# Performance work log

Measured on AMD Instinct MI355X. Metric: run time of the kernel, lower is better.

## Reference

```python
import jax, jax.numpy as jnp
import numpy as np

K = 16
N_BLOCKS = 3
EPS = 1e-5  # nn.BatchNorm2d default eps


def setup_inputs() -> dict:
    key = jax.random.key(0)
    ks = jax.random.split(key, 4)
    b, n, c_out = 8, 4096, 64
    s = 0.1
    return {
        "xyz": jax.random.normal(ks[0], (b, 3, n), dtype=jnp.float32),
        "w1": jax.random.normal(ks[1], (c_out, 3), dtype=jnp.float32) * s,
        "b1": jnp.zeros((c_out,), jnp.float32),
        "w2": jax.random.normal(ks[2], (c_out, c_out), dtype=jnp.float32) * s,
        "b2": jnp.zeros((c_out,), jnp.float32),
        "gamma": jnp.ones((c_out,), jnp.float32),
        "beta": jnp.zeros((c_out,), jnp.float32),
    }


def _forward(xyz, w1, b1, w2, b2, gamma, beta):
    pts = jnp.transpose(xyz, (0, 2, 1))  # (b, n, 3)
    sq = jnp.sum(pts * pts, axis=-1)     # (b, n)
    # dist[b, i, j] = ||pts[b, j] - pts[b, i]||^2  (gram trick, avoids (b,n,n,3))
    dist = sq[:, :, None] + sq[:, None, :] - 2.0 * jnp.einsum('bic,bjc->bij', pts, pts)
    # NOTE: torch.topk defaults to LARGEST values -- faithful to the source code,
    # which (perhaps unintentionally) selects the k+1 FARTHEST points.
    _, idx = jax.lax.top_k(dist, K + 1)  # (b, n, K+1)
    idx = idx[:, :, 1:]                  # drop first, dilation=1 -> (b, n, K)
    # gather neighbor coords: nbr[b, i, j] = pts[b, idx[b, i, j]]
    nbr = jax.vmap(lambda p, i: p[i])(pts, idx)      # (b, n, K, 3)
    rel = nbr - pts[:, :, None, :]                    # relative coords (b, n, K, 3)
    g = jnp.transpose(rel, (0, 3, 2, 1))              # (b, 3, K, n)
    for blk in range(N_BLOCKS):
        w, bb = (w1, b1) if blk == 0 else (w2, b2)
        g = jnp.einsum('oc,bckn->bokn', w, g) + bb[None, :, None, None]
        if blk == N_BLOCKS - 1:
            return jnp.max(g, axis=2)                 # (b, c_out, n)
        # self.bn is the BatchNorm2d module (truthy) so BN is always applied;
        # fresh torch module is in training mode -> batch statistics.
        mu = jnp.mean(g, axis=(0, 2, 3), keepdims=True)
        var = jnp.mean((g - mu) ** 2, axis=(0, 2, 3), keepdims=True)
        g = (g - mu) * jax.lax.rsqrt(var + EPS)
        g = g * gamma[None, :, None, None] + beta[None, :, None, None]
        g = jax.nn.relu(g)


def reference(xyz, w1, b1, w2, b2, gamma, beta):
    return _forward(xyz, w1, b1, w2, b2, gamma, beta)
```

## Files before the change

### kernel.cpp

```cpp
#include <hip/hip_runtime.h>

typedef unsigned int u32;
typedef unsigned short u16;
typedef unsigned long long u64;
typedef __attribute__((ext_vector_type(8))) short bf16x8;
typedef __attribute__((ext_vector_type(4))) float f32x4;

#define REL_OFF   0
#define PTS4_OFF  1572864
#define ACC_OFF   1703936
#define EXT_OFF   1705360
#define EXT_END   1713552


__device__ __forceinline__ u32 bfh(float v){
  u32 x = __float_as_uint(v);
  return (x + 0x7FFFu + ((x >> 16) & 1u)) >> 16;
}
__device__ __forceinline__ void split2(float v, u16* hh, u16* hl){
  u32 h = bfh(v);
  float hif = __uint_as_float(h << 16);
  u32 l = bfh(v - hif);
  *hh = (u16)h; *hl = (u16)l;
}
__device__ __forceinline__ u32 cvt_pk_bf16(float a, float b){
  u32 r;
  asm("v_cvt_pk_bf16_f32 %0, %1, %2" : "=v"(r) : "v"(a), "v"(b));
  return r;
}

template<int N>
__device__ __forceinline__ float dpp_ror_f(float x){
  int r = __builtin_amdgcn_update_dpp(__float_as_int(x), __float_as_int(x),
                                      0x120 + N, 0xf, 0xf, false);
  return __int_as_float(r);
}
__device__ __forceinline__ float row_sum16(float x){
  x += dpp_ror_f<1>(x);
  x += dpp_ror_f<2>(x);
  x += dpp_ror_f<4>(x);
  x += dpp_ror_f<8>(x);
  return x;
}
__device__ __forceinline__ float row_max16(float x){
  x = fmaxf(x, dpp_ror_f<1>(x));
  x = fmaxf(x, dpp_ror_f<2>(x));
  x = fmaxf(x, dpp_ror_f<4>(x));
  x = fmaxf(x, dpp_ror_f<8>(x));
  return x;
}

__global__ __launch_bounds__(256) void prep_kernel(const float* __restrict__ xyz,
                                                   float4* __restrict__ pts4,
                                                   float* __restrict__ mom,
                                                   const float* __restrict__ w2,
                                                   u16* __restrict__ w2h,
                                                   u16* __restrict__ w2l,
                                                   float* __restrict__ gsum32,
                                                   float* __restrict__ gsq32,
                                                   int do_w2){
#pragma clang fp contract(off)
  int g = blockIdx.x*256 + threadIdx.x;
  if (g < 16) mom[g] = 0.0f;
  if (do_w2){
    if (g < 4096) split2(w2[g], &w2h[g], &w2l[g]);
    if (g < 2048) gsum32[g] = 0.0f;
    else if (g < 4096) gsq32[g-2048] = 0.0f;
  }
  int b = g >> 12, n = g & 4095;
  const float* xb = xyz + (size_t)b*12288;
  float x = xb[n], y = xb[4096+n], z = xb[8192+n];
  float sq = (x*x + y*y) + z*z;
  pts4[g] = make_float4(x,y,z,sq);
}

__global__ void w2prep_kernel(const float* __restrict__ w2,
                              u16* __restrict__ w2h, u16* __restrict__ w2l,
                              float* __restrict__ gsum32, float* __restrict__ gsq32){
  int i = blockIdx.x*256 + threadIdx.x;
  split2(w2[i], &w2h[i], &w2l[i]);
  if (i < 2048) gsum32[i] = 0.0f; else gsq32[i-2048] = 0.0f;
}

template<int N>
__device__ __forceinline__ void chain_insert_n(double* s, double key){
  #pragma unroll
  for (int t = N-1; t >= 1; --t)
    s[t] = fmax(s[t], fmin(s[t-1], key));
  s[0] = fmax(s[0], key);
}

__global__ __launch_bounds__(256) void knn_kernel(const float4* __restrict__ pts4,
                                                  float* __restrict__ rel,
                                                  float* __restrict__ mom){
#pragma clang fp contract(off)
  __shared__ double ring[4352];
  __shared__ float bmom[16];
  __shared__ u32 gate[32];
  u32* lA = (u32*)ring;
  u16* lB = (u16*)((char*)ring + 18048);
  const int tid  = threadIdx.x;
  const int lane = tid & 63;
  const int wave = tid >> 6;
  const int q    = lane & 31;
  const int h    = lane >> 5;
  const int sp   = wave*2 + h;
  const int blk  = blockIdx.x;
  const int b    = blk >> 7;
  const int q0   = (blk & 127) << 5;
  const float4* __restrict__ P = pts4 + ((size_t)b << 12);
  const float4* __restrict__ C = P + (sp << 9);
  const float4 me = P[q0 + q];
  if (tid < 16) bmom[tid] = 0.0f;
  if (tid < 32) gate[tid] = 0u;
  __syncthreads();

  double s[17];
  #pragma unroll
  for (int i=0;i<17;i++) s[i] = 0.0;
  const int base = tid*17;
  const int jg0 = sp << 9;
  u32 wr = 0, rd = 0;
  double pD_ = 0.0;
  const double kinv = 1.52587890625e-05;

  #define KEY48(u, J) ({                                              \
    float dot_ = (me.x*c[(u)].x + me.y*c[(u)].y) + me.z*c[(u)].z;     \
    float d_   = (me.w + c[(u)].w) - 2.0f*dot_;                       \
    u32 ub_ = __float_as_uint(d_);                                    \
    ub_ ^= ((u32)(((int)ub_) >> 31) | 0x80000000u);                   \
    (double)ub_ * 65536.0 + (double)(4095 - (J)); })

  {
    float4 c[8];
    #pragma unroll
    for (int u=0;u<8;u++) c[u] = C[u];
    chain_insert_n<1>(s, KEY48(0, jg0+0));
    chain_insert_n<2>(s, KEY48(1, jg0+1));
    chain_insert_n<3>(s, KEY48(2, jg0+2));
    chain_insert_n<4>(s, KEY48(3, jg0+3));
    chain_insert_n<5>(s, KEY48(4, jg0+4));
    chain_insert_n<6>(s, KEY48(5, jg0+5));
    chain_insert_n<7>(s, KEY48(6, jg0+6));
    chain_insert_n<8>(s, KEY48(7, jg0+7));
  }
  {
    float4 c[8];
    #pragma unroll
    for (int u=0;u<8;u++) c[u] = C[8+u];
    chain_insert_n< 9>(s, KEY48(0, jg0+ 8));
    chain_insert_n<10>(s, KEY48(1, jg0+ 9));
    chain_insert_n<11>(s, KEY48(2, jg0+10));
    chain_insert_n<12>(s, KEY48(3, jg0+11));
    chain_insert_n<13>(s, KEY48(4, jg0+12));
    chain_insert_n<14>(s, KEY48(5, jg0+13));
    chain_insert_n<15>(s, KEY48(6, jg0+14));
    chain_insert_n<16>(s, KEY48(7, jg0+15));
  }
  {
    float4 c[8];
    #pragma unroll
    for (int u=0;u<8;u++) c[u] = C[16+u];
    #pragma unroll
    for (int u=0;u<8;u++) chain_insert_n<17>(s, KEY48(u, jg0+16+u));
  }

  u32 lastpub = (u32)(s[16] * kinv);
  atomicMax(&gate[q], lastpub);
  u32 ob = lastpub;

  #define INSERT_STEP() {                                        \
    bool act = rd != wr;                                         \
    double key = act ? pD_ : 0.0;                                \
    rd += act;                                                   \
    pD_ = ring[base + (int)(rd & 15u)];                          \
    if (__any(key > s[16])) chain_insert_n<17>(s, key);          \
  }

  for (int g8 = 24; g8 < 512; g8 += 8){
    if (__any((int)(wr - rd) >= 9)){
      do { INSERT_STEP(); } while (__any(rd != wr));
      ob = (u32)(s[16] * kinv);
      if (ob > lastpub){ atomicMax(&gate[q], ob); lastpub = ob; }
    }
    float4 c[8];
    #pragma unroll
    for (int u=0;u<8;u++) c[u] = C[g8 + u];
    const u32 mb = max(gate[q], ob);
    const u32 ib = (mb >> 31) ? (mb ^ 0x80000000u) : ~mb;
    const float gmin = __uint_as_float(ib);
    const u32 wr0 = wr;
    #pragma unroll
    for (int u=0;u<8;u++){
      const int j = jg0 + g8 + u;
      float dot = (me.x*c[u].x + me.y*c[u].y) + me.z*c[u].z;
      float d   = (me.w + c[u].w) - 2.0f*dot;
      if (d >= gmin){
        u32 ub = __float_as_uint(d);
        ub ^= ((u32)(((int)ub) >> 31) | 0x80000000u);
        ring[base + (int)(wr & 15u)] = (double)ub * 65536.0 + (double)(4095 - j);
        wr++;
      }
    }
    if (wr != wr0) pD_ = ring[base + (int)(rd & 15u)];
  }
  while (__any(rd != wr)) INSERT_STEP();
  #undef INSERT_STEP
  #undef KEY48

  __syncthreads();
  #pragma unroll
  for (int i=0;i<17;i++){
    const int o = (sp*17 + i)*33 + q;
    u32 hi = (u32)(s[i] * kinv);
    u32 lo = (u32)(s[i] - (double)hi * 65536.0);
    lA[o] = hi;
    lB[o] = (u16)lo;
  }
  __syncthreads();

  {
    const int mq  = tid >> 3;
    const int sub = tid & 7;
    const float4 qp = P[q0 + mq];
    float* __restrict__ ro = rel + (size_t)((b << 12) + q0 + mq) * 48;
    float sm0=0,sm1=0,sm2=0,sm3=0,sm4=0,sm5=0,sm6=0,sm7=0,sm8=0;
    int p = 0;
    for (int r=0;r<17;r++){
      const int idx = (sub*17 + p)*33 + mq;
      u64 mine = ((u64)lA[idx] << 16) | lB[idx];
      u64 kmax = mine;
      #pragma unroll
      for (int off=1; off<8; off<<=1){
        u64 o2 = __shfl_xor(kmax, off);
        kmax = (o2 > kmax) ? o2 : kmax;
      }
      p += (mine == kmax);
      if (r > 0 && sub == 0){
        const int j = 4095 - (int)(u32)(kmax & 0xFFFFull);
        const float4 nb = P[j];
        const float rx = nb.x - qp.x;
        const float ry = nb.y - qp.y;
        const float rz = nb.z - qp.z;
        ro[(r-1)*3+0] = rx; ro[(r-1)*3+1] = ry; ro[(r-1)*3+2] = rz;
        sm0 += rx; sm1 += ry; sm2 += rz;
        sm3 += rx*rx; sm4 += rx*ry; sm5 += rx*rz;
        sm6 += ry*ry; sm7 += ry*rz; sm8 += rz*rz;
      }
    }
    #pragma unroll
    for (int off=8; off<64; off<<=1){
      sm0 += __shfl_xor(sm0, off); sm1 += __shfl_xor(sm1, off); sm2 += __shfl_xor(sm2, off);
      sm3 += __shfl_xor(sm3, off); sm4 += __shfl_xor(sm4, off); sm5 += __shfl_xor(sm5, off);
      sm6 += __shfl_xor(sm6, off); sm7 += __shfl_xor(sm7, off); sm8 += __shfl_xor(sm8, off);
    }
    if (lane == 0){
      atomicAdd(&bmom[0], sm0); atomicAdd(&bmom[1], sm1); atomicAdd(&bmom[2], sm2);
      atomicAdd(&bmom[3], sm3); atomicAdd(&bmom[4], sm4); atomicAdd(&bmom[5], sm5);
      atomicAdd(&bmom[6], sm6); atomicAdd(&bmom[7], sm7); atomicAdd(&bmom[8], sm8);
    }
  }
  __syncthreads();
  if (tid < 9) atomicAdd(&mom[tid], bmom[tid]);
}

__device__ __noinline__ void stats1_to_lds(int o, const float* __restrict__ mom,
    const float* __restrict__ w1, const float* __restrict__ b1,
    const float* __restrict__ gamma, const float* __restrict__ beta,
    float* a1){
  const float Minv = 1.0f / 524288.0f;
  float m0 = mom[0]*Minv, m1 = mom[1]*Minv, m2 = mom[2]*Minv;
  float cxx = mom[3]*Minv - m0*m0;
  float cxy = mom[4]*Minv - m0*m1;
  float cxz = mom[5]*Minv - m0*m2;
  float cyy = mom[6]*Minv - m1*m1;
  float cyz = mom[7]*Minv - m1*m2;
  float czz = mom[8]*Minv - m2*m2;
  float wx = w1[o*3+0], wy = w1[o*3+1], wz = w1[o*3+2];
  float mu  = wx*m0 + wy*m1 + wz*m2 + b1[o];
  float var = wx*wx*cxx + wy*wy*cyy + wz*wz*czz
            + 2.0f*(wx*wy*cxy + wx*wz*cxz + wy*wz*cyz);
  float istd = rsqrtf(var + 1e-5f);
  float sc = gamma[o]*istd;
  float t1 = beta[o] - mu*sc;
  a1[o*4+0] = wx*sc;
  a1[o*4+1] = wy*sc;
  a1[o*4+2] = wz*sc;
  a1[o*4+3] = fmaf(sc, b1[o], t1);
}

__device__ __forceinline__ void stage_H_core(int e, int half,
    float rx, float ry, float rz, const float* a1, u16* Hh, u16* Hl){
  const float4* A1 = (const float4*)a1;
  const int ch0 = half*32;
  #pragma unroll
  for (int i=0;i<32;i+=4){
    float g[4];
    #pragma unroll
    for (int r2=0;r2<4;r2++){
      float4 a = A1[ch0+i+r2];
      float t = fmaf(a.x, rx, fmaf(a.y, ry, fmaf(a.z, rz, a.w)));
      g[r2] = fmaxf(t, 0.0f);
    }
    u32 h01 = cvt_pk_bf16(g[0], g[1]);
    u32 h23 = cvt_pk_bf16(g[2], g[3]);
    float l0 = g[0] - __uint_as_float(h01 << 16);
    float l1 = g[1] - __uint_as_float(h01 & 0xFFFF0000u);
    float l2 = g[2] - __uint_as_float(h23 << 16);
    float l3 = g[3] - __uint_as_float(h23 & 0xFFFF0000u);
    u32 l01 = cvt_pk_bf16(l0, l1);
    u32 l23 = cvt_pk_bf16(l2, l3);
    *(uint2*)&Hh[e*72 + ch0 + i] = make_uint2(h01, h23);
    *(uint2*)&Hl[e*72 + ch0 + i] = make_uint2(l01, l23);
  }
}

#define MFMA6(dst, b_h0, b_h1, b_l0, b_l1)                                   \
  dst = __builtin_amdgcn_mfma_f32_16x16x32_bf16(aH0, b_h0, dst, 0,0,0);      \
  dst = __builtin_amdgcn_mfma_f32_16x16x32_bf16(aH1, b_h1, dst, 0,0,0);      \
  dst = __builtin_amdgcn_mfma_f32_16x16x32_bf16(aH0, b_l0, dst, 0,0,0);      \
  dst = __builtin_amdgcn_mfma_f32_16x16x32_bf16(aH1, b_l1, dst, 0,0,0);      \
  dst = __builtin_amdgcn_mfma_f32_16x16x32_bf16(aL0, b_h0, dst, 0,0,0);      \
  dst = __builtin_amdgcn_mfma_f32_16x16x32_bf16(aL1, b_h1, dst, 0,0,0);

#define LOAD_W_FRAGS()                                                        \
  const int rA = (wave*16 + col)*64 + quad*8;                                 \
  bf16x8 aH0 = *(const bf16x8*)&w2h[rA];                                      \
  bf16x8 aH1 = *(const bf16x8*)&w2h[rA+32];                                   \
  bf16x8 aL0 = *(const bf16x8*)&w2l[rA];                                      \
  bf16x8 aL1 = *(const bf16x8*)&w2l[rA+32];

__global__ __launch_bounds__(256) void pass2_mfma(
    const float* __restrict__ rel,
    const float* __restrict__ mom, const float* __restrict__ w1,
    const float* __restrict__ b1, const float* __restrict__ gamma,
    const float* __restrict__ beta,
    const u16* __restrict__ w2h, const u16* __restrict__ w2l,
    const float* __restrict__ b2,
    float* __restrict__ gsum32, float* __restrict__ gsq32){
  __shared__ alignas(16) u16 Hh[128*72], Hl[128*72];
  __shared__ float a1s[256];
  const int tid = threadIdx.x, blk = blockIdx.x;
  const int e = tid>>1, half = tid&1;
  size_t eg = (size_t)blk*128 + e;
  const float rx = rel[eg*3+0], ry = rel[eg*3+1], rz = rel[eg*3+2];
  if (tid < 64) stats1_to_lds(tid, mom, w1, b1, gamma, beta, a1s);
  __syncthreads();
  stage_H_core(e, half, rx, ry, rz, (const float*)a1s, Hh, Hl);
  __syncthreads();
  const int lane = tid & 63, wave = tid >> 6;
  const int col = lane & 15, quad = lane >> 4;
  LOAD_W_FRAGS()
  float b2v[4];
  #pragma unroll
  for (int r=0;r<4;r++) b2v[r] = b2[wave*16 + quad*4 + r];
  float ssum[4] = {0,0,0,0}, ssq[4] = {0,0,0,0};
  #pragma unroll
  for (int nt=0; nt<8; nt++){
    const int offB = (nt*16 + col)*72 + quad*8;
    bf16x8 bH0 = *(const bf16x8*)&Hh[offB];
    bf16x8 bH1 = *(const bf16x8*)&Hh[offB+32];
    bf16x8 bL0 = *(const bf16x8*)&Hl[offB];
    bf16x8 bL1 = *(const bf16x8*)&Hl[offB+32];
    f32x4 a = {0.f,0.f,0.f,0.f};
    MFMA6(a, bH0, bH1, bL0, bL1)
    #pragma unroll
    for (int r=0;r<4;r++){
      float t = a[r] + b2v[r];
      ssum[r] += t; ssq[r] += t*t;
    }
  }
  #pragma unroll
  for (int r=0;r<4;r++){
    ssum[r] = row_sum16(ssum[r]);
    ssq[r]  = row_sum16(ssq[r]);
  }
  if (col == 0){
    const int st = (blk & 31)*64;
    #pragma unroll
    for (int r=0;r<4;r++){
      int ch = wave*16 + quad*4 + r;
      atomicAdd(&gsum32[st+ch], ssum[r]);
      atomicAdd(&gsq32[st+ch],  ssq[r]);
    }
  }
}

__global__ __launch_bounds__(256) void pass3_mfma(
    const float* __restrict__ rel,
    const float* __restrict__ mom, const float* __restrict__ w1,
    const float* __restrict__ b1, const float* __restrict__ gamma,
    const float* __restrict__ beta,
    const u16* __restrict__ w2h, const u16* __restrict__ w2l,
    const float* __restrict__ b2,
    const float* __restrict__ gsum32, const float* __restrict__ gsq32,
    float* __restrict__ out){
  __shared__ alignas(16) u16 Hh[128*72], Hl[128*72];
  __shared__ float a1s[256];
  __shared__ float s2s[64], c2s[64];
  const int tid = threadIdx.x, blk = blockIdx.x;
  const int e = tid>>1, half = tid&1;
  size_t eg = (size_t)blk*128 + e;
  const float rx = rel[eg*3+0], ry = rel[eg*3+1], rz = rel[eg*3+2];
  if (tid < 64){
    stats1_to_lds(tid, mom, w1, b1, gamma, beta, a1s);
  } else if (tid < 128){
    const int o = tid - 64;
    float s = 0.f, q = 0.f;
    #pragma unroll
    for (int i=0;i<32;i++){ s += gsum32[i*64+o]; q += gsq32[i*64+o]; }
    const float Minv = 1.0f / 524288.0f;
    float mu  = s*Minv;
    float var = q*Minv - mu*mu;
    float istd = rsqrtf(var + 1e-5f);
    float sc = gamma[o]*istd;
    float t2 = beta[o] - mu*sc;
    s2s[o] = sc;
    c2s[o] = fmaf(sc, b2[o], t2);
  }
  __syncthreads();
  stage_H_core(e, half, rx, ry, rz, (const float*)a1s, Hh, Hl);
  __syncthreads();
  const int lane = tid & 63, wave = tid >> 6;
  const int col = lane & 15, quad = lane >> 4;
  LOAD_W_FRAGS()
  float s2v[4], c2v[4], b2v[4];
  #pragma unroll
  for (int r=0;r<4;r++){
    int ch = wave*16 + quad*4 + r;
    s2v[r] = s2s[ch]; c2v[r] = c2s[ch]; b2v[r] = b2[ch];
  }
  f32x4 acc[8];
  #pragma unroll
  for (int nt=0; nt<8; nt++){
    const int offB = (nt*16 + col)*72 + quad*8;
    bf16x8 bH0 = *(const bf16x8*)&Hh[offB];
    bf16x8 bH1 = *(const bf16x8*)&Hh[offB+32];
    bf16x8 bL0 = *(const bf16x8*)&Hl[offB];
    bf16x8 bL1 = *(const bf16x8*)&Hl[offB+32];
    f32x4 a = {0.f,0.f,0.f,0.f};
    MFMA6(a, bH0, bH1, bL0, bL1)
    acc[nt] = a;
  }
  __syncthreads();
  #pragma unroll
  for (int nt=0; nt<8; nt++){
    const int eo = nt*16 + col;
    const int ch0 = wave*16 + quad*4;
    float h0, h1, h2, h3;
    {
      float g0 = acc[nt][0] + b2v[0];
      float g1 = acc[nt][1] + b2v[1];
      float g2 = acc[nt][2] + b2v[2];
      float g3 = acc[nt][3] + b2v[3];
      h0 = fmaxf(fmaf(g0, s2v[0], c2v[0]), 0.0f);
      h1 = fmaxf(fmaf(g1, s2v[1], c2v[1]), 0.0f);
      h2 = fmaxf(fmaf(g2, s2v[2], c2v[2]), 0.0f);
      h3 = fmaxf(fmaf(g3, s2v[3], c2v[3]), 0.0f);
    }
    u32 h01 = cvt_pk_bf16(h0, h1);
    u32 h23 = cvt_pk_bf16(h2, h3);
    float l0 = h0 - __uint_as_float(h01 << 16);
    float l1 = h1 - __uint_as_float(h01 & 0xFFFF0000u);
    float l2 = h2 - __uint_as_float(h23 << 16);
    float l3 = h3 - __uint_as_float(h23 & 0xFFFF0000u);
    u32 l01 = cvt_pk_bf16(l0, l1);
    u32 l23 = cvt_pk_bf16(l2, l3);
    *(uint2*)&Hh[eo*72 + ch0] = make_uint2(h01, h23);
    *(uint2*)&Hl[eo*72 + ch0] = make_uint2(l01, l23);
  }
  __syncthreads();
  #pragma unroll
  for (int nt=0; nt<8; nt++){
    const int offB = (nt*16 + col)*72 + quad*8;
    bf16x8 bH0 = *(const bf16x8*)&Hh[offB];
    bf16x8 bH1 = *(const bf16x8*)&Hh[offB+32];
    bf16x8 bL0 = *(const bf16x8*)&Hl[offB];
    bf16x8 bL1 = *(const bf16x8*)&Hl[offB+32];
    f32x4 a = {0.f,0.f,0.f,0.f};
    MFMA6(a, bH0, bH1, bL0, bL1)
    acc[nt][0] = row_max16(a[0]+b2v[0]);
    acc[nt][1] = row_max16(a[1]+b2v[1]);
    acc[nt][2] = row_max16(a[2]+b2v[2]);
    acc[nt][3] = row_max16(a[3]+b2v[3]);
  }
  if (col == 0){
    const int bb = blk >> 9;
    const int n0 = (blk & 511) * 8;
    #pragma unroll
    for (int r=0;r<4;r++){
      const int ch = wave*16 + quad*4 + r;
      float* po = out + (((size_t)bb*64 + ch) << 12) + n0;
      f32x4 v0 = {acc[0][r], acc[1][r], acc[2][r], acc[3][r]};
      f32x4 v1 = {acc[4][r], acc[5][r], acc[6][r], acc[7][r]};
      *(f32x4*)po = v0;
      *((f32x4*)po + 1) = v1;
    }
  }
}

extern "C" void kernel_launch(void* const* d_in, const int* in_sizes, int n_in,
                              void* d_out, int out_size, void* d_ws, size_t ws_size,
                              hipStream_t stream){
  const float* xyz   = (const float*)d_in[0];
  const float* w1    = (const float*)d_in[1];
  const float* b1    = (const float*)d_in[2];
  const float* w2    = (const float*)d_in[3];
  const float* b2    = (const float*)d_in[4];
  const float* gamma = (const float*)d_in[5];
  const float* beta  = (const float*)d_in[6];
  float* out = (float*)d_out;
  float* ws  = (float*)d_ws;

  float*  rel    = ws + REL_OFF;
  float4* pts4   = (float4*)(ws + PTS4_OFF);
  float*  mom    = ws + ACC_OFF;

  const bool big = ws_size >= (size_t)EXT_END * sizeof(float);
  u16 *w2h, *w2l; float *gsum32, *gsq32;
  if (big){
    w2h    = (u16*)(ws + EXT_OFF);
    w2l    = (u16*)(ws + EXT_OFF + 2048);
    gsum32 = ws + EXT_OFF + 4096;
    gsq32  = ws + EXT_OFF + 6144;
  } else {
    w2h    = (u16*)(ws + PTS4_OFF);
    w2l    = (u16*)(ws + PTS4_OFF + 2048);
    gsum32 = ws + PTS4_OFF + 4096;
    gsq32  = ws + PTS4_OFF + 6144;
  }

  prep_kernel  <<<128,  256, 0, stream>>>(xyz, pts4, mom, w2, w2h, w2l,
                                          gsum32, gsq32, big ? 1 : 0);
  knn_kernel   <<<1024, 256, 0, stream>>>(pts4, rel, mom);
  if (!big)
    w2prep_kernel<<<16, 256, 0, stream>>>(w2, w2h, w2l, gsum32, gsq32);
  pass2_mfma   <<<4096, 256, 0, stream>>>(rel, mom, w1, b1, gamma, beta,
                                          w2h, w2l, b2, gsum32, gsq32);
  pass3_mfma   <<<4096, 256, 0, stream>>>(rel, mom, w1, b1, gamma, beta,
                                          w2h, w2l, b2, gsum32, gsq32, out);
}
```

Measured before the change: 267.5 us.

## Fuse BN-stats and output passes into one persistent kernel with grid barrier

```diff
diff --git a/kernel.cpp b/kernel.cpp
--- a/kernel.cpp
+++ b/kernel.cpp
@@ -11,7 +11,6 @@
 #define ACC_OFF   1703936
 #define EXT_OFF   1705360
 #define EXT_END   1713552
-
 
 __device__ __forceinline__ u32 bfh(float v){
   u32 x = __float_as_uint(v);
@@ -48,6 +47,19 @@
   x = fmaxf(x, dpp_ror_f<4>(x));
   x = fmaxf(x, dpp_ror_f<8>(x));
   return x;
+}
+
+__device__ __forceinline__ void grid_barrier(u32* cnt, u32 expected){
+  __syncthreads();
+  if (threadIdx.x == 0){
+    __threadfence();
+    atomicAdd(cnt, 1u);
+    while (__hip_atomic_load(cnt, __ATOMIC_ACQUIRE, __HIP_MEMORY_SCOPE_AGENT)
+           < expected)
+      __builtin_amdgcn_s_sleep(2);
+    __threadfence();
+  }
+  __syncthreads();
 }
 
 __global__ __launch_bounds__(256) void prep_kernel(const float* __restrict__ xyz,
@@ -58,10 +70,12 @@
                                                    u16* __restrict__ w2l,
                                                    float* __restrict__ gsum32,
                                                    float* __restrict__ gsq32,
+                                                   u32* __restrict__ cnt,
                                                    int do_w2){
 #pragma clang fp contract(off)
   int g = blockIdx.x*256 + threadIdx.x;
   if (g < 16) mom[g] = 0.0f;
+  if (g >= 16 && g < 18) cnt[g-16] = 0u;
   if (do_w2){
     if (g < 4096) split2(w2[g], &w2h[g], &w2l[g]);
     if (g < 2048) gsum32[g] = 0.0f;
@@ -289,6 +303,23 @@
   a1[o*4+3] = fmaf(sc, b1[o], t1);
 }
 
+__device__ __forceinline__ void stats2_to_lds(int o,
+    const float* __restrict__ gsum32, const float* __restrict__ gsq32,
+    const float* __restrict__ b2, const float* __restrict__ gamma,
+    const float* __restrict__ beta, float* s2s, float* c2s){
+  float s = 0.f, q = 0.f;
+  #pragma unroll
+  for (int i=0;i<32;i++){ s += gsum32[i*64+o]; q += gsq32[i*64+o]; }
+  const float Minv = 1.0f / 524288.0f;
+  float mu  = s*Minv;
+  float var = q*Minv - mu*mu;
+  float istd = rsqrtf(var + 1e-5f);
+  float sc = gamma[o]*istd;
+  float t2 = beta[o] - mu*sc;
+  s2s[o] = sc;
+  c2s[o] = fmaf(sc, b2[o], t2);
+}
+
 __device__ __forceinline__ void stage_H_core(int e, int half,
     float rx, float ry, float rz, const float* a1, u16* Hh, u16* Hl){
   const float4* A1 = (const float4*)a1;
@@ -330,23 +361,16 @@
   bf16x8 aL0 = *(const bf16x8*)&w2l[rA];                                      \
   bf16x8 aL1 = *(const bf16x8*)&w2l[rA+32];
 
-__global__ __launch_bounds__(256) void pass2_mfma(
-    const float* __restrict__ rel,
-    const float* __restrict__ mom, const float* __restrict__ w1,
-    const float* __restrict__ b1, const float* __restrict__ gamma,
-    const float* __restrict__ beta,
+__device__ __forceinline__ void pass2_tile(int blk, int tid,
+    const float* __restrict__ rel, const float* a1s,
     const u16* __restrict__ w2h, const u16* __restrict__ w2l,
     const float* __restrict__ b2,
-    float* __restrict__ gsum32, float* __restrict__ gsq32){
-  __shared__ alignas(16) u16 Hh[128*72], Hl[128*72];
-  __shared__ float a1s[256];
-  const int tid = threadIdx.x, blk = blockIdx.x;
+    float* __restrict__ gsum32, float* __restrict__ gsq32,
+    u16* Hh, u16* Hl){
   const int e = tid>>1, half = tid&1;
   size_t eg = (size_t)blk*128 + e;
   const float rx = rel[eg*3+0], ry = rel[eg*3+1], rz = rel[eg*3+2];
-  if (tid < 64) stats1_to_lds(tid, mom, w1, b1, gamma, beta, a1s);
-  __syncthreads();
-  stage_H_core(e, half, rx, ry, rz, (const float*)a1s, Hh, Hl);
+  stage_H_core(e, half, rx, ry, rz, a1s, Hh, Hl);
   __syncthreads();
   const int lane = tid & 63, wave = tid >> 6;
   const int col = lane & 15, quad = lane >> 4;
@@ -384,42 +408,19 @@
       atomicAdd(&gsq32[st+ch],  ssq[r]);
     }
   }
-}
-
-__global__ __launch_bounds__(256) void pass3_mfma(
-    const float* __restrict__ rel,
-    const float* __restrict__ mom, const float* __restrict__ w1,
-    const float* __restrict__ b1, const float* __restrict__ gamma,
-    const float* __restrict__ beta,
+  __syncthreads();
+}
+
+__device__ __forceinline__ void pass3_tile(int blk, int tid,
+    const float* __restrict__ rel, const float* a1s,
+    const float* s2s, const float* c2s,
     const u16* __restrict__ w2h, const u16* __restrict__ w2l,
-    const float* __restrict__ b2,
-    const float* __restrict__ gsum32, const float* __restrict__ gsq32,
-    float* __restrict__ out){
-  __shared__ alignas(16) u16 Hh[128*72], Hl[128*72];
-  __shared__ float a1s[256];
-  __shared__ float s2s[64], c2s[64];
-  const int tid = threadIdx.x, blk = blockIdx.x;
+    const float* __restrict__ b2, float* __restrict__ out,
+    u16* Hh, u16* Hl){
   const int e = tid>>1, half = tid&1;
   size_t eg = (size_t)blk*128 + e;
   const float rx = rel[eg*3+0], ry = rel[eg*3+1], rz = rel[eg*3+2];
-  if (tid < 64){
-    stats1_to_lds(tid, mom, w1, b1, gamma, beta, a1s);
-  } else if (tid < 128){
-    const int o = tid - 64;
-    float s = 0.f, q = 0.f;
-    #pragma unroll
-    for (int i=0;i<32;i++){ s += gsum32[i*64+o]; q += gsq32[i*64+o]; }
-    const float Minv = 1.0f / 524288.0f;
-    float mu  = s*Minv;
-    float var = q*Minv - mu*mu;
-    float istd = rsqrtf(var + 1e-5f);
-    float sc = gamma[o]*istd;
-    float t2 = beta[o] - mu*sc;
-    s2s[o] = sc;
-    c2s[o] = fmaf(sc, b2[o], t2);
-  }
-  __syncthreads();
-  stage_H_core(e, half, rx, ry, rz, (const float*)a1s, Hh, Hl);
+  stage_H_core(e, half, rx, ry, rz, a1s, Hh, Hl);
   __syncthreads();
   const int lane = tid & 63, wave = tid >> 6;
   const int col = lane & 15, quad = lane >> 4;
@@ -497,6 +498,69 @@
       *((f32x4*)po + 1) = v1;
     }
   }
+  __syncthreads();
+}
+
+__global__ __launch_bounds__(256) void pass2_mfma(
+    const float* __restrict__ rel,
+    const float* __restrict__ mom, const float* __restrict__ w1,
+    const float* __restrict__ b1, const float* __restrict__ gamma,
+    const float* __restrict__ beta,
+    const u16* __restrict__ w2h, const u16* __restrict__ w2l,
+    const float* __restrict__ b2,
+    float* __restrict__ gsum32, float* __restrict__ gsq32){
+  __shared__ alignas(16) u16 Hh[128*72], Hl[128*72];
+  __shared__ float a1s[256];
+  const int tid = threadIdx.x;
+  if (tid < 64) stats1_to_lds(tid, mom, w1, b1, gamma, beta, a1s);
+  __syncthreads();
+  pass2_tile(blockIdx.x, tid, rel, a1s, w2h, w2l, b2, gsum32, gsq32, Hh, Hl);
+}
+
+__global__ __launch_bounds__(256) void pass3_mfma(
+    const float* __restrict__ rel,
+    const float* __restrict__ mom, const float* __restrict__ w1,
+    const float* __restrict__ b1, const float* __restrict__ gamma,
+    const float* __restrict__ beta,
+    const u16* __restrict__ w2h, const u16* __restrict__ w2l,
+    const float* __restrict__ b2,
+    const float* __restrict__ gsum32, const float* __restrict__ gsq32,
+    float* __restrict__ out){
+  __shared__ alignas(16) u16 Hh[128*72], Hl[128*72];
+  __shared__ float a1s[256];
+  __shared__ float s2s[64], c2s[64];
+  const int tid = threadIdx.x;
+  if (tid < 64) stats1_to_lds(tid, mom, w1, b1, gamma, beta, a1s);
+  else if (tid < 128) stats2_to_lds(tid-64, gsum32, gsq32, b2, gamma, beta, s2s, c2s);
+  __syncthreads();
+  pass3_tile(blockIdx.x, tid, rel, a1s, s2s, c2s, w2h, w2l, b2, out, Hh, Hl);
+}
+
+__global__ __launch_bounds__(256) void fused_pass(
+    const float* __restrict__ rel,
+    const float* __restrict__ mom, const float* __restrict__ w1,
+    const float* __restrict__ b1, const float* __restrict__ gamma,
+    const float* __restrict__ beta,
+    const u16* __restrict__ w2h, const u16* __restrict__ w2l,
+    const float* __restrict__ b2,
+    float* __restrict__ gsum32, float* __restrict__ gsq32,
+    float* __restrict__ out, u32* __restrict__ cnt){
+  __shared__ alignas(16) u16 Hh[128*72], Hl[128*72];
+  __shared__ float a1s[256];
+  __shared__ float s2s[64], c2s[64];
+  const int tid = threadIdx.x, bid = blockIdx.x;
+  if (tid < 64) stats1_to_lds(tid, mom, w1, b1, gamma, beta, a1s);
+  __syncthreads();
+  #pragma unroll 1
+  for (int t=0; t<4; t++)
+    pass2_tile(t*1024 + bid, tid, rel, a1s, w2h, w2l, b2, gsum32, gsq32, Hh, Hl);
+  grid_barrier(cnt, 1024u);
+  if (tid >= 64 && tid < 128)
+    stats2_to_lds(tid-64, gsum32, gsq32, b2, gamma, beta, s2s, c2s);
+  __syncthreads();
+  #pragma unroll 1
+  for (int t=0; t<4; t++)
+    pass3_tile(t*1024 + bid, tid, rel, a1s, s2s, c2s, w2h, w2l, b2, out, Hh, Hl);
 }
 
 extern "C" void kernel_launch(void* const* d_in, const int* in_sizes, int n_in,
@@ -515,6 +579,7 @@
   float*  rel    = ws + REL_OFF;
   float4* pts4   = (float4*)(ws + PTS4_OFF);
   float*  mom    = ws + ACC_OFF;
+  u32*    cnt    = (u32*)(ws + ACC_OFF + 16);
 
   const bool big = ws_size >= (size_t)EXT_END * sizeof(float);
   u16 *w2h, *w2l; float *gsum32, *gsq32;
@@ -530,13 +595,23 @@
     gsq32  = ws + PTS4_OFF + 6144;
   }
 
+  int nb = 0;
+  hipError_t oe = hipOccupancyMaxActiveBlocksPerMultiprocessor(&nb, fused_pass, 256, 0);
+  const bool fuse = (oe == hipSuccess) && (nb >= 4);
+
   prep_kernel  <<<128,  256, 0, stream>>>(xyz, pts4, mom, w2, w2h, w2l,
-                                          gsum32, gsq32, big ? 1 : 0);
+                                          gsum32, gsq32, cnt, big ? 1 : 0);
   knn_kernel   <<<1024, 256, 0, stream>>>(pts4, rel, mom);
   if (!big)
     w2prep_kernel<<<16, 256, 0, stream>>>(w2, w2h, w2l, gsum32, gsq32);
-  pass2_mfma   <<<4096, 256, 0, stream>>>(rel, mom, w1, b1, gamma, beta,
+
+  if (fuse){
+    fused_pass <<<1024, 256, 0, stream>>>(rel, mom, w1, b1, gamma, beta,
+                                          w2h, w2l, b2, gsum32, gsq32, out, cnt);
+  } else {
+    pass2_mfma <<<4096, 256, 0, stream>>>(rel, mom, w1, b1, gamma, beta,
                                           w2h, w2l, b2, gsum32, gsq32);
-  pass3_mfma   <<<4096, 256, 0, stream>>>(rel, mom, w1, b1, gamma, beta,
+    pass3_mfma <<<4096, 256, 0, stream>>>(rel, mom, w1, b1, gamma, beta,
                                           w2h, w2l, b2, gsum32, gsq32, out);
-}
+  }
+}
```

New measurement: 266.3 us. No clear change (-0.5%).
